# Performance work log

Measured on AMD Instinct MI355X. Metric: run time of the kernel, lower is better.

The kernel has to match this reference:

```python
import jax, jax.numpy as jnp
import numpy as np

B, S, D, H, F, V, T, L = 64, 1024, 256, 256, 128, 50000, 64, 8
H2 = 2 * H
DIN = H2 + D + 3 * F  # 1152


def setup_inputs() -> dict:
    key = jax.random.key(0)
    ks = jax.random.split(key, 12)
    sd = 0.05
    return {
        "word_ids": jax.random.randint(ks[0], (B, S), 1, V, dtype=jnp.int32),
        "embed": jax.random.normal(ks[1], (V, D), jnp.float32) * sd,
        "encoder_outputs": jax.random.normal(ks[2], (B, S, H2), jnp.float32) * sd,
        "wconv1": jax.random.normal(ks[3], (F, 1, D), jnp.float32) * sd,
        "bconv1": jax.random.normal(ks[4], (F,), jnp.float32) * sd,
        "wconv2": jax.random.normal(ks[5], (F, 2, D), jnp.float32) * sd,
        "bconv2": jax.random.normal(ks[6], (F,), jnp.float32) * sd,
        "wconv3": jax.random.normal(ks[7], (F, 3, D), jnp.float32) * sd,
        "bconv3": jax.random.normal(ks[8], (F,), jnp.float32) * sd,
        "W_ih": jax.random.normal(ks[9], (4 * H2, DIN), jnp.float32) * sd,
        "W_hh": jax.random.normal(ks[10], (4 * H2, H2), jnp.float32) * sd,
        "W_fc": jax.random.normal(ks[11], (T, H2), jnp.float32) * sd,
        "seg_len": L,
    }


def reference(word_ids, embed, encoder_outputs, wconv1, bconv1, wconv2, bconv2,
              wconv3, bconv3, W_ih, W_hh, W_fc, seg_len):
    b, s = word_ids.shape
    d = embed.shape[1]
    h2 = encoder_outputs.shape[-1]
    h = h2 // 2
    nseg = s // seg_len

    # word features via embedding lookup (WordFeature with single 'word' feature)
    wf = embed[word_ids]                                  # [B, S, D]
    xs = wf.reshape(b, nseg, seg_len, d)                  # [B, nseg, L, D]
    c_w = xs.mean(axis=2)                                 # [B, nseg, D]
    es = encoder_outputs.reshape(b, nseg, seg_len, h2)
    c_h = es.mean(axis=2)                                 # [B, nseg, 2H]

    # char-CNN per segment: conv2d(1->F, (fs, D)) == 1D conv over time with D in-channels
    xc = xs.reshape(b * nseg, seg_len, d).transpose(0, 2, 1)  # [N, D, L]

    def conv_pool(w, bias):
        k = w.transpose(0, 2, 1)                          # [F, D, fs]
        y = jax.lax.conv_general_dilated(xc, k, window_strides=(1,),
                                         padding="VALID",
                                         dimension_numbers=("NCH", "OIH", "NCH"))
        y = jax.nn.relu(y + bias[None, :, None])
        return y.max(axis=2)                              # max-pool over time -> [N, F]

    c_x = jnp.concatenate([conv_pool(wconv1, bconv1),
                           conv_pool(wconv2, bconv2),
                           conv_pool(wconv3, bconv3)], axis=1)
    c_x = c_x.reshape(b, nseg, -1)                        # [B, nseg, 3F]

    dec_in = jnp.concatenate([c_w, c_h, c_x], axis=-1)    # [B, nseg, DIN]

    # decoder init: fwd-last / bwd-first encoder states
    h0 = jnp.concatenate([encoder_outputs[:, -1, :h], encoder_outputs[:, 0, h:]], axis=1)
    c0 = jnp.zeros_like(h0)

    def step(carry, x):
        hh, cc = carry
        gates = x @ W_ih.T + hh @ W_hh.T                  # [B, 4*2H]
        i, fg, g, o = jnp.split(gates, 4, axis=1)
        cc = jax.nn.sigmoid(fg) * cc + jax.nn.sigmoid(i) * jnp.tanh(g)
        hh = jax.nn.sigmoid(o) * jnp.tanh(cc)
        out = jax.nn.log_softmax(hh @ W_fc.T, axis=-1)
        return (hh, cc), out

    _, outs = jax.lax.scan(step, (h0, c0), dec_in.transpose(1, 0, 2))  # [nseg, B, T]
    return outs.transpose(1, 0, 2).reshape(b * nseg, -1)  # batch-major like the torch loop
```

## Files before the change

### kernel.cpp

```cpp
#include <hip/hip_runtime.h>
#include <math.h>

#define BB   64
#define SS   1024
#define DD   256
#define H2   512
#define FF   128
#define TT   64
#define NSEG 128
#define DIN  1152
#define G4   2048
#define MROWS 8192
#define MX   65536

typedef __attribute__((ext_vector_type(8))) short bf16x8;
typedef __attribute__((ext_vector_type(4))) float f32x4;

__device__ __forceinline__ unsigned short f2b(float f){
    union { float f; unsigned u; } v; v.f = f;
    unsigned r = v.u + 0x7fffu + ((v.u >> 16) & 1u);
    return (unsigned short)(r >> 16);
}
__device__ __forceinline__ float b2f(unsigned short h){
    union { unsigned u; float f; } v; v.u = ((unsigned)h) << 16;
    return v.f;
}
__device__ __forceinline__ float fsig(float x){
    return 1.f / (1.f + __expf(-x));
}
__device__ __forceinline__ float ftanh(float x){
    float e = __expf(-2.f * fabsf(x));
    float r = (1.f - e) / (1.f + e);
    return x < 0.f ? -r : r;
}


__global__ void k_cvt(const float* __restrict__ src, unsigned short* __restrict__ dst, int n){
    int i = blockIdx.x * 256 + threadIdx.x;
    if (i < n) dst[i] = f2b(src[i]);
}

__global__ void k_wf(const float* __restrict__ w1, const float* __restrict__ w2,
                     const float* __restrict__ w3, unsigned short* __restrict__ Wf){
    int i = blockIdx.x * 256 + threadIdx.x;
    int col = i >> 8, d = i & 255;
    float v;
    if (col < 128)      v = w1[col * 256 + d];
    else if (col < 384) { int f = (col - 128) & 127; int tap = (col - 128) >> 7; v = w2[f * 512 + tap * 256 + d]; }
    else                { int c = col - 384; int f = c & 127; int tap = c >> 7;  v = w3[f * 768 + tap * 256 + d]; }
    Wf[i] = f2b(v);
}

__global__ void k_tr_wfc(const float* __restrict__ src, float* __restrict__ dst){
    int i = blockIdx.x * 256 + threadIdx.x;
    int v = i >> 9, k = i & 511;
    dst[k * 64 + v] = src[i];
}

__global__ void k_gather(const int* __restrict__ wid, const float* __restrict__ embed,
                         unsigned short* __restrict__ X){
    int i = blockIdx.x * 256 + threadIdx.x;
    int row = i >> 6, d4 = i & 63;
    int w = wid[row];
    float4 v = *(const float4*)(embed + (size_t)w * DD + d4 * 4);
    ushort4 o; o.x = f2b(v.x); o.y = f2b(v.y); o.z = f2b(v.z); o.w = f2b(v.w);
    *(ushort4*)(X + (size_t)row * DD + d4 * 4) = o;
}

__global__ void k_cw(const unsigned short* __restrict__ X, unsigned short* __restrict__ dec){
    int i = blockIdx.x * 256 + threadIdx.x;
    int row = i >> 8, d = i & 255;
    const unsigned short* p = X + (size_t)row * 8 * DD + d;
    float s = 0.f;
#pragma unroll
    for (int t = 0; t < 8; t++) s += b2f(p[t * DD]);
    dec[(size_t)row * DIN + d] = f2b(s * 0.125f);
}

__global__ void k_ch(const float* __restrict__ enc, unsigned short* __restrict__ dec){
    int i = blockIdx.x * 256 + threadIdx.x;
    int row = i >> 9, c = i & 511;
    const float* p = enc + (size_t)row * 8 * H2 + c;
    float s = 0.f;
#pragma unroll
    for (int t = 0; t < 8; t++) s += p[t * H2];
    dec[(size_t)row * DIN + 256 + c] = f2b(s * 0.125f);
}

__global__ void k_h0(const float* __restrict__ enc, unsigned short* __restrict__ Hbuf){
    int i = blockIdx.x * 256 + threadIdx.x;
    int b = i >> 9, c = i & 511;
    float v = (c < 256) ? enc[(size_t)b * SS * H2 + (size_t)(SS - 1) * H2 + c]
                        : enc[(size_t)b * SS * H2 + c];
    v = fminf(fmaxf(v, -1.875f), 1.875f);
    Hbuf[(size_t)b * 512 + c] = f2b(v);
}

__global__ void k_fill(uint4* __restrict__ p){
    int i = blockIdx.x * 256 + threadIdx.x;
    uint4 v; v.x = v.y = v.z = v.w = 0x7FC07FC0u;
    p[i] = v;
}

__global__ __launch_bounds__(256) void gemm_bt(
    const unsigned short* __restrict__ A, const unsigned short* __restrict__ Bm,
    unsigned short* __restrict__ C, int M, int N, int K)
{
    __shared__ unsigned short As[128][40];
    __shared__ unsigned short Bs[128][40];
    const int tid = threadIdx.x;
    const int m0 = blockIdx.y * 128, n0 = blockIdx.x * 128;
    const int w = tid >> 6, lane = tid & 63;
    const int lm = lane & 15, quad = lane >> 4;
    const int wm = (w >> 1) * 64, wn = (w & 1) * 64;

    const f32x4 z = {0.f, 0.f, 0.f, 0.f};
    f32x4 acc[4][4];
#pragma unroll
    for (int i = 0; i < 4; i++)
#pragma unroll
        for (int j = 0; j < 4; j++) acc[i][j] = z;

    const int r0 = tid >> 2;
    const int kp = (tid & 3) * 8;

    for (int kc = 0; kc < K; kc += 32){
        uint4 a0 = *(const uint4*)(A + (size_t)(m0 + r0) * K + kc + kp);
        uint4 a1 = *(const uint4*)(A + (size_t)(m0 + 64 + r0) * K + kc + kp);
        uint4 b0 = *(const uint4*)(Bm + (size_t)(n0 + r0) * K + kc + kp);
        uint4 b1 = *(const uint4*)(Bm + (size_t)(n0 + 64 + r0) * K + kc + kp);
        __syncthreads();
        *(uint4*)&As[r0][kp] = a0;
        *(uint4*)&As[64 + r0][kp] = a1;
        *(uint4*)&Bs[r0][kp] = b0;
        *(uint4*)&Bs[64 + r0][kp] = b1;
        __syncthreads();
        bf16x8 af[4], bf[4];
#pragma unroll
        for (int mt = 0; mt < 4; mt++) af[mt] = *(const bf16x8*)&As[wm + mt * 16 + lm][quad * 8];
#pragma unroll
        for (int nt = 0; nt < 4; nt++) bf[nt] = *(const bf16x8*)&Bs[wn + nt * 16 + lm][quad * 8];
#pragma unroll
        for (int mt = 0; mt < 4; mt++)
#pragma unroll
            for (int nt = 0; nt < 4; nt++)
                acc[mt][nt] = __builtin_amdgcn_mfma_f32_16x16x32_bf16(af[mt], bf[nt], acc[mt][nt], 0, 0, 0);
    }
#pragma unroll
    for (int mt = 0; mt < 4; mt++){
        int mrow = m0 + wm + mt * 16 + quad * 4;
#pragma unroll
        for (int nt = 0; nt < 4; nt++){
            int ncol = n0 + wn + nt * 16 + lm;
#pragma unroll
            for (int r = 0; r < 4; r++)
                C[(size_t)(mrow + r) * N + ncol] = f2b(acc[mt][nt][r]);
        }
    }
}

__global__ __launch_bounds__(256) void gemm_bt_gates(
    const unsigned short* __restrict__ A, const unsigned short* __restrict__ Bm,
    unsigned short* __restrict__ C, int M, int N, int K)
{
    __shared__ unsigned short As[128][40];
    __shared__ unsigned short Bs[128][40];
    const int tid = threadIdx.x;
    const int m0 = blockIdx.y * 128, n0 = blockIdx.x * 128;
    const int w = tid >> 6, lane = tid & 63;
    const int lm = lane & 15, quad = lane >> 4;
    const int wm = (w >> 1) * 64, wn = (w & 1) * 64;

    const f32x4 z = {0.f, 0.f, 0.f, 0.f};
    f32x4 acc[4][4];
#pragma unroll
    for (int i = 0; i < 4; i++)
#pragma unroll
        for (int j = 0; j < 4; j++) acc[i][j] = z;

    const int r0 = tid >> 2;
    const int kp = (tid & 3) * 8;

    for (int kc = 0; kc < K; kc += 32){
        uint4 a0 = *(const uint4*)(A + (size_t)(m0 + r0) * K + kc + kp);
        uint4 a1 = *(const uint4*)(A + (size_t)(m0 + 64 + r0) * K + kc + kp);
        uint4 b0 = *(const uint4*)(Bm + (size_t)(n0 + r0) * K + kc + kp);
        uint4 b1 = *(const uint4*)(Bm + (size_t)(n0 + 64 + r0) * K + kc + kp);
        __syncthreads();
        *(uint4*)&As[r0][kp] = a0;
        *(uint4*)&As[64 + r0][kp] = a1;
        *(uint4*)&Bs[r0][kp] = b0;
        *(uint4*)&Bs[64 + r0][kp] = b1;
        __syncthreads();
        bf16x8 af[4], bf[4];
#pragma unroll
        for (int mt = 0; mt < 4; mt++) af[mt] = *(const bf16x8*)&As[wm + mt * 16 + lm][quad * 8];
#pragma unroll
        for (int nt = 0; nt < 4; nt++) bf[nt] = *(const bf16x8*)&Bs[wn + nt * 16 + lm][quad * 8];
#pragma unroll
        for (int mt = 0; mt < 4; mt++)
#pragma unroll
            for (int nt = 0; nt < 4; nt++)
                acc[mt][nt] = __builtin_amdgcn_mfma_f32_16x16x32_bf16(af[mt], bf[nt], acc[mt][nt], 0, 0, 0);
    }
#pragma unroll
    for (int mt = 0; mt < 4; mt++){
        int mrow = m0 + wm + mt * 16 + quad * 4;
#pragma unroll
        for (int nt = 0; nt < 4; nt++){
            int ncol = n0 + wn + nt * 16 + lm;
            int g = ncol >> 9, c = ncol & 511;
            int gb = c >> 5, hcl = c & 31;
            int n = hcl * 4 + g;
#pragma unroll
            for (int r = 0; r < 4; r++){
                int m = mrow + r;
                int b = m >> 7, t = m & 127;
                int grp = b >> 4, bl = b & 15;
                size_t dst = (((size_t)(grp * 16 + gb) * NSEG + t) * 128 + n) * 16 + bl;
                C[dst] = f2b(acc[mt][nt][r]);
            }
        }
    }
}

__global__ void k_pool(const unsigned short* __restrict__ G, const float* __restrict__ bias,
                       unsigned short* __restrict__ dec, int taps, int colofs){
    int i = blockIdx.x * 256 + threadIdx.x;
    int row = i >> 7, f = i & 127;
    int N = taps * 128;
    float mx = -1e30f;
    for (int t = 0; t <= 8 - taps; t++){
        float a = 0.f;
        for (int tap = 0; tap < taps; tap++)
            a += b2f(G[(size_t)(row * 8 + t + tap) * N + tap * 128 + f]);
        mx = fmaxf(mx, a);
    }
    mx = fmaxf(mx + bias[f], 0.f);
    dec[(size_t)row * DIN + 768 + colofs + f] = f2b(mx);
}

__global__ __launch_bounds__(512, 2) void k_lstm(
    const unsigned short* __restrict__ gxt,
    const unsigned short* __restrict__ Whh,
    unsigned short* __restrict__ Hbuf)
{
    __shared__ unsigned short h_lds[2][16 * 512];

    const int tid = threadIdx.x;
    const int nb = blockIdx.x;
    const int grp = nb >> 4, gb = nb & 15;
    const int w = tid >> 6, lane = tid & 63, lm = lane & 15, quad = lane >> 4;
    const int g = lm & 3;

    bf16x8 wf[16];
    {
        int n = w * 16 + lm;
        const unsigned short* p = Whh + (size_t)((n & 3) * 512 + gb * 32 + (n >> 2)) * H2 + quad * 8;
#pragma unroll
        for (int ks = 0; ks < 16; ks++) wf[ks] = *(const bf16x8*)(p + ks * 32);
    }

    float cst[4] = {0.f, 0.f, 0.f, 0.f};

    union Chunk { unsigned long long q[2]; uint4 u4; };

    for (int t = 0; t < NSEG; t++){
#pragma unroll
        for (int ks = 0; ks < 16; ks++) asm volatile("" : "+v"(wf[ks]));

        const unsigned short* hsrc = Hbuf + (size_t)t * (BB * H2) + (size_t)grp * (16 * H2);
        Chunk ch[2];
#pragma unroll
        for (int j = 0; j < 2; j++){
            const unsigned long long* p = (const unsigned long long*)(hsrc + (size_t)(j * 512 + tid) * 8);
            ch[j].q[0] = __hip_atomic_load(p,     __ATOMIC_RELAXED, __HIP_MEMORY_SCOPE_AGENT);
            ch[j].q[1] = __hip_atomic_load(p + 1, __ATOMIC_RELAXED, __HIP_MEMORY_SCOPE_AGENT);
        }

        const unsigned short* gchunk = gxt + ((size_t)nb * NSEG + t) * 2048;
        ushort4 pr = *(const ushort4*)(gchunk + (w * 16 + lm) * 16 + quad * 4);

        unsigned pend = 0x3u;
        while (pend){
            unsigned np = 0;
#pragma unroll
            for (int j = 0; j < 2; j++){
                if (pend & (1u << j)){
                    if (((ch[j].q[0] | ch[j].q[1]) & 0x4000400040004000ULL) != 0ULL){
                        const unsigned long long* p = (const unsigned long long*)(hsrc + (size_t)(j * 512 + tid) * 8);
                        ch[j].q[0] = __hip_atomic_load(p,     __ATOMIC_RELAXED, __HIP_MEMORY_SCOPE_AGENT);
                        ch[j].q[1] = __hip_atomic_load(p + 1, __ATOMIC_RELAXED, __HIP_MEMORY_SCOPE_AGENT);
                        np |= 1u << j;
                    }
                }
            }
            pend = np;
            if (pend) __builtin_amdgcn_s_sleep(1);
        }

        char* hb = (char*)&h_lds[t & 1][0];
#pragma unroll
        for (int j = 0; j < 2; j++){
            unsigned addr = (unsigned)(j * 512 + tid) * 16u;
            addr ^= ((addr >> 10) & 7u) << 4;
            *(uint4*)(hb + addr) = ch[j].u4;
        }
        __syncthreads();

        const unsigned hrowb = (unsigned)lm << 10;
        const unsigned swz = (unsigned)(lm & 7) << 4;
        f32x4 acc = {0.f, 0.f, 0.f, 0.f};
#pragma unroll
        for (int ks = 0; ks < 16; ks++){
            unsigned colb = ((unsigned)ks << 6) + ((unsigned)quad << 4);
            bf16x8 avv = *(const bf16x8*)(hb + ((hrowb + colb) ^ swz));
            acc = __builtin_amdgcn_mfma_f32_16x16x32_bf16(avv, wf[ks], acc, 0, 0, 0);
        }

        const unsigned short* prs = (const unsigned short*)&pr;
        unsigned short hv4[4];
#pragma unroll
        for (int r = 0; r < 4; r++){
            float a = acc[r] + b2f(prs[r]);
            float bsw = __shfl_xor(a, 1);
            float p  = (g & 1) ? bsw : a;
            float qq = (g & 1) ? a : bsw;
            float c2 = __shfl_xor(p, 2);
            float d2 = __shfl_xor(qq, 2);
            float iv = (g & 2) ? c2 : p;
            float gv = (g & 2) ? p  : c2;
            float fv = (g & 2) ? d2 : qq;
            float ov = (g & 2) ? qq : d2;
            float si = fsig(iv), sf = fsig(fv), so = fsig(ov);
            float cn = sf * cst[r] + si * ftanh(gv);
            cst[r] = cn;
            unsigned short hv = f2b(so * ftanh(cn));
            if (hv & 0x4000u) hv = 0;
            hv4[r] = hv;
        }

#pragma unroll
        for (int r = 0; r < 4; r++){
            unsigned v01 = (unsigned)hv4[r] | ((unsigned)(unsigned short)__shfl_xor((int)hv4[r], 4) << 16);
            unsigned v23 = (unsigned)__shfl_xor((int)v01, 8);
            unsigned long long outq = (unsigned long long)v01 | ((unsigned long long)v23 << 32);
            if (lm == 0){
                int bt = grp * 16 + quad * 4 + r;
                unsigned long long* dp = (unsigned long long*)
                    (Hbuf + (size_t)(t + 1) * (BB * H2) + (size_t)bt * H2 + gb * 32 + w * 4);
                __hip_atomic_store(dp, outq, __ATOMIC_RELAXED, __HIP_MEMORY_SCOPE_AGENT);
            }
        }
        asm volatile("" ::: "memory");
    }
}

__global__ __launch_bounds__(256) void k_out(
    const unsigned short* __restrict__ Hbuf, const float* __restrict__ Wt, float* __restrict__ out)
{
    __shared__ float hsh[4][H2];
    const int w = threadIdx.x >> 6, lane = threadIdx.x & 63;
    const int row = blockIdx.x * 4 + w;
    const int b = row >> 7, t = row & 127;
    const unsigned short* hp = Hbuf + (size_t)(t + 1) * (BB * H2) + (size_t)b * H2;
    uint4 hv = *(const uint4*)(hp + lane * 8);
    const unsigned short* hs = (const unsigned short*)&hv;
#pragma unroll
    for (int i = 0; i < 8; i++) hsh[w][lane * 8 + i] = b2f(hs[i]);
    __syncthreads();
    float acc = 0.f;
#pragma unroll 8
    for (int k = 0; k < H2; k++)
        acc = fmaf(hsh[w][k], Wt[k * 64 + lane], acc);
    float m = acc;
#pragma unroll
    for (int off = 32; off; off >>= 1) m = fmaxf(m, __shfl_xor(m, off));
    float e = expf(acc - m), s = e;
#pragma unroll
    for (int off = 32; off; off >>= 1) s += __shfl_xor(s, off);
    out[(size_t)row * TT + lane] = acc - m - logf(s);
}

extern "C" void kernel_launch(void* const* d_in, const int* in_sizes, int n_in,
                              void* d_out, int out_size, void* d_ws, size_t ws_size,
                              hipStream_t stream)
{
    const int*   wid = (const int*)d_in[0];
    const float* emb = (const float*)d_in[1];
    const float* enc = (const float*)d_in[2];
    const float* wc1 = (const float*)d_in[3];
    const float* bc1 = (const float*)d_in[4];
    const float* wc2 = (const float*)d_in[5];
    const float* bc2 = (const float*)d_in[6];
    const float* wc3 = (const float*)d_in[7];
    const float* bc3 = (const float*)d_in[8];
    const float* wih = (const float*)d_in[9];
    const float* whh = (const float*)d_in[10];
    const float* wfc = (const float*)d_in[11];

    char* ws = (char*)d_ws;
    size_t off = 0;
    auto alloc = [&](size_t bytes) -> void* {
        void* p = ws + off; off += (bytes + 255) & ~(size_t)255; return p;
    };
    unsigned short* X    = (unsigned short*)alloc((size_t)MX * DD * 2);
    unsigned short* dec  = (unsigned short*)alloc((size_t)MROWS * DIN * 2);
    unsigned short* Gb   = (unsigned short*)alloc((size_t)MX * 384 * 2);
    unsigned short* Wfb  = (unsigned short*)alloc((size_t)768 * 256 * 2);
    unsigned short* Wihb = (unsigned short*)alloc((size_t)G4 * DIN * 2);
    unsigned short* Whhb = (unsigned short*)alloc((size_t)G4 * H2 * 2);
    float*          Wfct = (float*)alloc((size_t)H2 * TT * 4);
    unsigned short* Hbuf  = X;
    unsigned short* gates = Gb;

    k_cvt<<<(G4 * DIN + 255) / 256, 256, 0, stream>>>(wih, Wihb, G4 * DIN);
    k_cvt<<<(G4 * H2 + 255) / 256, 256, 0, stream>>>(whh, Whhb, G4 * H2);
    k_wf<<<768, 256, 0, stream>>>(wc1, wc2, wc3, Wfb);
    k_tr_wfc<<<128, 256, 0, stream>>>(wfc, Wfct);
    k_gather<<<MX / 4, 256, 0, stream>>>(wid, emb, X);
    k_cw<<<MROWS, 256, 0, stream>>>(X, dec);
    k_ch<<<MROWS * 2, 256, 0, stream>>>(enc, dec);

    gemm_bt<<<dim3(1, 512), 256, 0, stream>>>(X, Wfb,                         Gb, MX, 128, 256);
    k_pool<<<4096, 256, 0, stream>>>(Gb, bc1, dec, 1, 0);
    gemm_bt<<<dim3(2, 512), 256, 0, stream>>>(X, Wfb + (size_t)128 * 256,     Gb, MX, 256, 256);
    k_pool<<<4096, 256, 0, stream>>>(Gb, bc2, dec, 2, 128);
    gemm_bt<<<dim3(3, 512), 256, 0, stream>>>(X, Wfb + (size_t)384 * 256,     Gb, MX, 384, 256);
    k_pool<<<4096, 256, 0, stream>>>(Gb, bc3, dec, 3, 256);

    k_h0<<<BB * H2 / 256, 256, 0, stream>>>(enc, Hbuf);
    k_fill<<<2048, 256, 0, stream>>>((uint4*)(Hbuf + BB * H2));

    gemm_bt_gates<<<dim3(16, 64), 256, 0, stream>>>(dec, Wihb, gates, MROWS, G4, DIN);
    k_lstm<<<64, 512, 0, stream>>>(gates, Whhb, Hbuf);
    k_out<<<2048, 256, 0, stream>>>(Hbuf, Wfct, (float*)d_out);
}
```

Baseline: 1.098 ms.

## Fuse char-CNN conv GEMMs with max-pool epilogue; split LSTM MFMA accumulator chain

Replaces three conv GEMMs plus three pooling kernels with one kernel that computes the conv as shifted-row GEMM accumulation over taps and applies bias, ReLU and the time max-pool in registers before writing directly into the decoder input. This removes the intermediate Gb buffer round trip and five kernel launches. The LSTM recurrence also uses two independent MFMA accumulators to shorten the dependent MFMA chain per step. The fused kernel reloads X rows once per tap, and the clamped row index handles tile overflow at the end of the buffer.

Result: faster. 1.060 ms (-3.5%).

```diff
diff --git a/kernel.cpp b/kernel.cpp
--- a/kernel.cpp
+++ b/kernel.cpp
@@ -102,7 +102,88 @@
     p[i] = v;
 }
 
-__global__ __launch_bounds__(256) void gemm_bt(
+__global__ __launch_bounds__(256) void gemm_conv_pool(
+    const unsigned short* __restrict__ X, const unsigned short* __restrict__ Wf,
+    const float* __restrict__ b1, const float* __restrict__ b2, const float* __restrict__ b3,
+    unsigned short* __restrict__ dec)
+{
+    __shared__ unsigned short As[128][40];
+    __shared__ unsigned short Bs[128][40];
+    const int tid = threadIdx.x;
+    const int m0 = blockIdx.x * 128;
+    const int w = tid >> 6, lane = tid & 63;
+    const int lm = lane & 15, quad = lane >> 4;
+    const int wm = (w >> 1) * 64, wn = (w & 1) * 64;
+    const int r0 = tid >> 2;
+    const int kp = (tid & 3) * 8;
+
+    const int woffs[3]  = {0, 128, 384};
+    const int colofs[3] = {0, 128, 256};
+    const float* biases[3] = {b1, b2, b3};
+
+    for (int c = 0; c < 3; c++){
+        const int taps = c + 1;
+        const f32x4 z = {0.f, 0.f, 0.f, 0.f};
+        f32x4 acc[4][4];
+#pragma unroll
+        for (int i = 0; i < 4; i++)
+#pragma unroll
+            for (int j = 0; j < 4; j++) acc[i][j] = z;
+
+        for (int kc2 = 0; kc2 < taps * 256; kc2 += 32){
+            int tap = kc2 >> 8, kc = kc2 & 255;
+            int ra = m0 + r0 + tap;        if (ra > MX - 1) ra = MX - 1;
+            int rb = m0 + 64 + r0 + tap;   if (rb > MX - 1) rb = MX - 1;
+            int bw = woffs[c] + tap * 128;
+            uint4 a0 = *(const uint4*)(X  + (size_t)ra * DD + kc + kp);
+            uint4 a1 = *(const uint4*)(X  + (size_t)rb * DD + kc + kp);
+            uint4 b0 = *(const uint4*)(Wf + (size_t)(bw + r0) * DD + kc + kp);
+            uint4 b1v= *(const uint4*)(Wf + (size_t)(bw + 64 + r0) * DD + kc + kp);
+            __syncthreads();
+            *(uint4*)&As[r0][kp] = a0;
+            *(uint4*)&As[64 + r0][kp] = a1;
+            *(uint4*)&Bs[r0][kp] = b0;
+            *(uint4*)&Bs[64 + r0][kp] = b1v;
+            __syncthreads();
+            bf16x8 af[4], bf[4];
+#pragma unroll
+            for (int mt = 0; mt < 4; mt++) af[mt] = *(const bf16x8*)&As[wm + mt * 16 + lm][quad * 8];
+#pragma unroll
+            for (int nt = 0; nt < 4; nt++) bf[nt] = *(const bf16x8*)&Bs[wn + nt * 16 + lm][quad * 8];
+#pragma unroll
+            for (int mt = 0; mt < 4; mt++)
+#pragma unroll
+                for (int nt = 0; nt < 4; nt++)
+                    acc[mt][nt] = __builtin_amdgcn_mfma_f32_16x16x32_bf16(af[mt], bf[nt], acc[mt][nt], 0, 0, 0);
+        }
+
+        const int pmax = 8 - taps;
+        const float* bias = biases[c];
+#pragma unroll
+        for (int nt = 0; nt < 4; nt++){
+            int f = wn + nt * 16 + lm;
+            float bv = bias[f];
+#pragma unroll
+            for (int mt = 0; mt < 4; mt++){
+                float mx = -1e30f;
+#pragma unroll
+                for (int r = 0; r < 4; r++){
+                    int p = (quad & 1) * 4 + r;
+                    if (p <= pmax) mx = fmaxf(mx, acc[mt][nt][r]);
+                }
+                float po = __shfl_xor(mx, 16);
+                mx = fmaxf(mx, po);
+                if (!(quad & 1)){
+                    int seg = (m0 >> 3) + (wm >> 3) + mt * 2 + (quad >> 1);
+                    float o = fmaxf(mx + bv, 0.f);
+                    dec[(size_t)seg * DIN + 768 + colofs[c] + f] = f2b(o);
+                }
+            }
+        }
+    }
+}
+
+__global__ __launch_bounds__(256) void gemm_bt_gates(
     const unsigned short* __restrict__ A, const unsigned short* __restrict__ Bm,
     unsigned short* __restrict__ C, int M, int N, int K)
 {
@@ -152,63 +233,6 @@
 #pragma unroll
         for (int nt = 0; nt < 4; nt++){
             int ncol = n0 + wn + nt * 16 + lm;
-#pragma unroll
-            for (int r = 0; r < 4; r++)
-                C[(size_t)(mrow + r) * N + ncol] = f2b(acc[mt][nt][r]);
-        }
-    }
-}
-
-__global__ __launch_bounds__(256) void gemm_bt_gates(
-    const unsigned short* __restrict__ A, const unsigned short* __restrict__ Bm,
-    unsigned short* __restrict__ C, int M, int N, int K)
-{
-    __shared__ unsigned short As[128][40];
-    __shared__ unsigned short Bs[128][40];
-    const int tid = threadIdx.x;
-    const int m0 = blockIdx.y * 128, n0 = blockIdx.x * 128;
-    const int w = tid >> 6, lane = tid & 63;
-    const int lm = lane & 15, quad = lane >> 4;
-    const int wm = (w >> 1) * 64, wn = (w & 1) * 64;
-
-    const f32x4 z = {0.f, 0.f, 0.f, 0.f};
-    f32x4 acc[4][4];
-#pragma unroll
-    for (int i = 0; i < 4; i++)
-#pragma unroll
-        for (int j = 0; j < 4; j++) acc[i][j] = z;
-
-    const int r0 = tid >> 2;
-    const int kp = (tid & 3) * 8;
-
-    for (int kc = 0; kc < K; kc += 32){
-        uint4 a0 = *(const uint4*)(A + (size_t)(m0 + r0) * K + kc + kp);
-        uint4 a1 = *(const uint4*)(A + (size_t)(m0 + 64 + r0) * K + kc + kp);
-        uint4 b0 = *(const uint4*)(Bm + (size_t)(n0 + r0) * K + kc + kp);
-        uint4 b1 = *(const uint4*)(Bm + (size_t)(n0 + 64 + r0) * K + kc + kp);
-        __syncthreads();
-        *(uint4*)&As[r0][kp] = a0;
-        *(uint4*)&As[64 + r0][kp] = a1;
-        *(uint4*)&Bs[r0][kp] = b0;
-        *(uint4*)&Bs[64 + r0][kp] = b1;
-        __syncthreads();
-        bf16x8 af[4], bf[4];
-#pragma unroll
-        for (int mt = 0; mt < 4; mt++) af[mt] = *(const bf16x8*)&As[wm + mt * 16 + lm][quad * 8];
-#pragma unroll
-        for (int nt = 0; nt < 4; nt++) bf[nt] = *(const bf16x8*)&Bs[wn + nt * 16 + lm][quad * 8];
-#pragma unroll
-        for (int mt = 0; mt < 4; mt++)
-#pragma unroll
-            for (int nt = 0; nt < 4; nt++)
-                acc[mt][nt] = __builtin_amdgcn_mfma_f32_16x16x32_bf16(af[mt], bf[nt], acc[mt][nt], 0, 0, 0);
-    }
-#pragma unroll
-    for (int mt = 0; mt < 4; mt++){
-        int mrow = m0 + wm + mt * 16 + quad * 4;
-#pragma unroll
-        for (int nt = 0; nt < 4; nt++){
-            int ncol = n0 + wn + nt * 16 + lm;
             int g = ncol >> 9, c = ncol & 511;
             int gb = c >> 5, hcl = c & 31;
             int n = hcl * 4 + g;
@@ -224,23 +248,8 @@
     }
 }
 
-__global__ void k_pool(const unsigned short* __restrict__ G, const float* __restrict__ bias,
-                       unsigned short* __restrict__ dec, int taps, int colofs){
-    int i = blockIdx.x * 256 + threadIdx.x;
-    int row = i >> 7, f = i & 127;
-    int N = taps * 128;
-    float mx = -1e30f;
-    for (int t = 0; t <= 8 - taps; t++){
-        float a = 0.f;
-        for (int tap = 0; tap < taps; tap++)
-            a += b2f(G[(size_t)(row * 8 + t + tap) * N + tap * 128 + f]);
-        mx = fmaxf(mx, a);
-    }
-    mx = fmaxf(mx + bias[f], 0.f);
-    dec[(size_t)row * DIN + 768 + colofs + f] = f2b(mx);
-}
-
-__global__ __launch_bounds__(512, 2) void k_lstm(
+__global__ __attribute__((amdgpu_flat_work_group_size(512, 512), amdgpu_waves_per_eu(2, 2)))
+void k_lstm(
     const unsigned short* __restrict__ gxt,
     const unsigned short* __restrict__ Whh,
     unsigned short* __restrict__ Hbuf)
@@ -310,19 +319,22 @@
 
         const unsigned hrowb = (unsigned)lm << 10;
         const unsigned swz = (unsigned)(lm & 7) << 4;
-        f32x4 acc = {0.f, 0.f, 0.f, 0.f};
-#pragma unroll
-        for (int ks = 0; ks < 16; ks++){
-            unsigned colb = ((unsigned)ks << 6) + ((unsigned)quad << 4);
-            bf16x8 avv = *(const bf16x8*)(hb + ((hrowb + colb) ^ swz));
-            acc = __builtin_amdgcn_mfma_f32_16x16x32_bf16(avv, wf[ks], acc, 0, 0, 0);
+        f32x4 acc0 = {0.f, 0.f, 0.f, 0.f}, acc1 = {0.f, 0.f, 0.f, 0.f};
+#pragma unroll
+        for (int ks = 0; ks < 16; ks += 2){
+            unsigned colb0 = ((unsigned)ks << 6) + ((unsigned)quad << 4);
+            unsigned colb1 = colb0 + 64u;
+            bf16x8 av0 = *(const bf16x8*)(hb + ((hrowb + colb0) ^ swz));
+            bf16x8 av1 = *(const bf16x8*)(hb + ((hrowb + colb1) ^ swz));
+            acc0 = __builtin_amdgcn_mfma_f32_16x16x32_bf16(av0, wf[ks],     acc0, 0, 0, 0);
+            acc1 = __builtin_amdgcn_mfma_f32_16x16x32_bf16(av1, wf[ks + 1], acc1, 0, 0, 0);
         }
 
         const unsigned short* prs = (const unsigned short*)&pr;
         unsigned short hv4[4];
 #pragma unroll
         for (int r = 0; r < 4; r++){
-            float a = acc[r] + b2f(prs[r]);
+            float a = acc0[r] + acc1[r] + b2f(prs[r]);
             float bsw = __shfl_xor(a, 1);
             float p  = (g & 1) ? bsw : a;
             float qq = (g & 1) ? a : bsw;
@@ -422,12 +434,7 @@
     k_cw<<<MROWS, 256, 0, stream>>>(X, dec);
     k_ch<<<MROWS * 2, 256, 0, stream>>>(enc, dec);
 
-    gemm_bt<<<dim3(1, 512), 256, 0, stream>>>(X, Wfb,                         Gb, MX, 128, 256);
-    k_pool<<<4096, 256, 0, stream>>>(Gb, bc1, dec, 1, 0);
-    gemm_bt<<<dim3(2, 512), 256, 0, stream>>>(X, Wfb + (size_t)128 * 256,     Gb, MX, 256, 256);
-    k_pool<<<4096, 256, 0, stream>>>(Gb, bc2, dec, 2, 128);
-    gemm_bt<<<dim3(3, 512), 256, 0, stream>>>(X, Wfb + (size_t)384 * 256,     Gb, MX, 384, 256);
-    k_pool<<<4096, 256, 0, stream>>>(Gb, bc3, dec, 3, 256);
+    gemm_conv_pool<<<512, 256, 0, stream>>>(X, Wfb, bc1, bc2, bc3, dec);
 
     k_h0<<<BB * H2 / 256, 256, 0, stream>>>(enc, Hbuf);
     k_fill<<<2048, 256, 0, stream>>>((uint4*)(Hbuf + BB * H2));
```
